# Kernel optimization log

Measured on AMD Instinct MI355X. Metric: run time of the kernel, lower is better.

The kernel has to match this reference:

```python
import jax, jax.numpy as jnp
import numpy as np

D = 192
HEADS = 4
HD = D // HEADS
R = 3  # correlation radius actually used in forward_level
NDISP = (2 * R + 1) ** 2  # 49
T = 3  # frames -> 2 consecutive pairs
ITERS = 4


def layer_norm(x, w, b, eps=1e-5):
    m = jnp.mean(x, axis=-1, keepdims=True)
    v = jnp.var(x, axis=-1, keepdims=True)
    return (x - m) / jnp.sqrt(v + eps) * w + b


def mha(x, in_w, in_b, out_w, out_b):
    # torch nn.MultiheadAttention, batch_first, self-attention
    B, N, _ = x.shape
    qkv = x @ in_w.T + in_b
    q, k, v = jnp.split(qkv, 3, axis=-1)
    q = q.reshape(B, N, HEADS, HD).transpose(0, 2, 1, 3) * (1.0 / float(np.sqrt(HD)))
    k = k.reshape(B, N, HEADS, HD).transpose(0, 2, 1, 3)
    v = v.reshape(B, N, HEADS, HD).transpose(0, 2, 1, 3)
    att = jax.nn.softmax(jnp.einsum('bhqd,bhkd->bhqk', q, k), axis=-1)
    y = jnp.einsum('bhqk,bhkd->bhqd', att, v).transpose(0, 2, 1, 3).reshape(B, N, D)
    return y @ out_w.T + out_b


def tblock(x, p):
    ln1w, ln1b, inw, inb, ow, ob, ln2w, ln2b, w1, b1, w2, b2 = p
    x = x + mha(layer_norm(x, ln1w, ln1b), inw, inb, ow, ob)
    h = layer_norm(x, ln2w, ln2b)
    h = jax.nn.gelu(h @ w1.T + b1, approximate=False) @ w2.T + b2
    return x + h


def local_corr(f1, f2):
    C = f1.shape[1]
    scale = 1.0 / float(np.sqrt(C))
    outs = []
    for dy in range(-R, R + 1):
        for dx in range(-R, R + 1):
            f2s = jnp.roll(f2, (dy, dx), axis=(2, 3))
            outs.append(jnp.sum(f1 * f2s, axis=1) * scale)
    return jnp.stack(outs, axis=1)


def grid_sample_bilinear_border(img, grid):
    # img: B,C,H,W; grid: B,Ho,Wo,2 with (x,y) in [-1,1]; align_corners=True, border padding
    B, C, H, W = img.shape
    x = jnp.clip((grid[..., 0] + 1.0) * 0.5 * (W - 1), 0.0, W - 1)
    y = jnp.clip((grid[..., 1] + 1.0) * 0.5 * (H - 1), 0.0, H - 1)
    x0 = jnp.floor(x); y0 = jnp.floor(y)
    x1 = jnp.minimum(x0 + 1, W - 1); y1 = jnp.minimum(y0 + 1, H - 1)
    wx = (x - x0)[:, None]; wy = (y - y0)[:, None]
    imgf = img.reshape(B, C, H * W)
    Ho, Wo = x.shape[1], x.shape[2]
    def gather(yy, xx):
        idx = (yy * W + xx).astype(jnp.int32).reshape(B, 1, Ho * Wo)
        return jnp.take_along_axis(imgf, idx, axis=2).reshape(B, C, Ho, Wo)
    v00 = gather(y0, x0); v01 = gather(y0, x1)
    v10 = gather(y1, x0); v11 = gather(y1, x1)
    return v00 * (1 - wx) * (1 - wy) + v01 * wx * (1 - wy) + v10 * (1 - wx) * wy + v11 * wx * wy


def warp(img, flow):
    # flow in pixels, Bx2xHxW
    B, C, H, W = img.shape
    xs = jnp.linspace(-1.0, 1.0, W); ys = jnp.linspace(-1.0, 1.0, H)
    gx, gy = jnp.meshgrid(xs, ys)  # each (H, W), 'xy' indexing
    base = jnp.stack([gx, gy], axis=-1)[None]
    off = jnp.stack([flow[:, 0] * (2.0 / max(W - 1, 1)),
                     flow[:, 1] * (2.0 / max(H - 1, 1))], axis=-1)
    return grid_sample_bilinear_border(img, base + off)


def upsample2x_align(img):
    # F.interpolate(scale_factor=2, mode='bilinear', align_corners=True)
    B, C, H, W = img.shape
    Ho, Wo = 2 * H, 2 * W
    xs = jnp.linspace(-1.0, 1.0, Wo); ys = jnp.linspace(-1.0, 1.0, Ho)
    gx, gy = jnp.meshgrid(xs, ys)
    grid = jnp.broadcast_to(jnp.stack([gx, gy], axis=-1)[None], (B, Ho, Wo, 2))
    return grid_sample_bilinear_border(img, grid)


def conv2d(x, w, b):
    y = jax.lax.conv_general_dilated(x, w, (1, 1), ((1, 1), (1, 1)),
                                     dimension_numbers=('NCHW', 'OIHW', 'NCHW'))
    return y + b[None, :, None, None]


def _forward(feats_l1, feats_l2, feats_l3, tok_w, tok_b,
             lcm_ln1_w, lcm_ln1_b, lcm_in_w, lcm_in_b, lcm_out_w, lcm_out_b,
             lcm_ln2_w, lcm_ln2_b, lcm_mlp_w1, lcm_mlp_b1, lcm_mlp_w2, lcm_mlp_b2,
             gtr_ln1_w, gtr_ln1_b, gtr_in_w, gtr_in_b, gtr_out_w, gtr_out_b,
             gtr_ln2_w, gtr_ln2_b, gtr_mlp_w1, gtr_mlp_b1, gtr_mlp_w2, gtr_mlp_b2,
             head_w1, head_b1, head_w2, head_b2,
             ref1_w1, ref1_b1, ref1_w2, ref1_b2,
             ref0_w1, ref0_b1, ref0_w2, ref0_b2):
    feats = [[feats_l1[t] for t in range(T)],
             [feats_l2[t] for t in range(T)],
             [feats_l3[t] for t in range(T)]]
    # ---- CostTokenizer ----
    tokens = []
    for lvl in range(3):
        toks = []
        for k in range(T - 1):
            corr = local_corr(feats[lvl][k], feats[lvl][k + 1])
            toks.append(jnp.einsum('bchw,dc->bdhw', corr, tok_w[lvl]) + tok_b[lvl][None, :, None, None])
        tokens.append(toks)
    lcm_p = [(lcm_ln1_w[i], lcm_ln1_b[i], lcm_in_w[i], lcm_in_b[i], lcm_out_w[i], lcm_out_b[i],
              lcm_ln2_w[i], lcm_ln2_b[i], lcm_mlp_w1[i], lcm_mlp_b1[i], lcm_mlp_w2[i], lcm_mlp_b2[i])
             for i in range(lcm_ln1_w.shape[0])]
    gtr_p = [(gtr_ln1_w[i], gtr_ln1_b[i], gtr_in_w[i], gtr_in_b[i], gtr_out_w[i], gtr_out_b[i],
              gtr_ln2_w[i], gtr_ln2_b[i], gtr_mlp_w1[i], gtr_mlp_b1[i], gtr_mlp_w2[i], gtr_mlp_b2[i])
             for i in range(gtr_ln1_w.shape[0])]
    # ---- LatentCostMemory (EMA state; .detach() -> stop_gradient; state resets when N changes) ----
    state = None
    latent = []
    for toks in tokens:
        lvl_lat = []
        for tok in toks:
            B_, Dd, H, W = tok.shape
            x = tok.reshape(B_, Dd, H * W).transpose(0, 2, 1)  # b (h w) d
            for p in lcm_p:
                x = tblock(x, p)
            if state is None or state.shape[1] != x.shape[1]:
                state = jax.lax.stop_gradient(x)
            x = 0.8 * x + 0.2 * state
            state = jax.lax.stop_gradient(x)
            lvl_lat.append(x.transpose(0, 2, 1))  # b d n
        latent.append(lvl_lat)
    H8, W8 = feats[1][0].shape[-2:]
    coarse = []
    for lat in latent[1]:
        x = lat.transpose(0, 2, 1)
        for p in gtr_p:
            x = tblock(x, p)
        fv = jax.nn.gelu(x @ head_w1.T + head_b1, approximate=False) @ head_w2.T + head_b2
        coarse.append(fv.transpose(0, 2, 1).reshape(-1, 2, H8, W8))
    # ---- MSRecurrentDecoder ----
    outs = []
    for k, f8 in enumerate(coarse):
        cur = f8
        for _ in range(ITERS):
            w10 = warp(feats[1][k + 1], cur)
            x = jnp.concatenate([feats[1][k], cur, w10], axis=1)
            cur = cur + conv2d(jax.nn.gelu(conv2d(x, ref1_w1, ref1_b1), approximate=False), ref1_w2, ref1_b2)
        cur2 = upsample2x_align(cur)
        for _ in range(ITERS):
            w10 = warp(feats[0][k + 1], cur2)
            x = jnp.concatenate([feats[0][k], cur2, w10], axis=1)
            cur2 = cur2 + conv2d(jax.nn.gelu(conv2d(x, ref0_w1, ref0_b1), approximate=False), ref0_w2, ref0_b2)
        outs.append(cur2)
    return jnp.stack(outs)  # [pairs, B, 2, H/4, W/4]


def setup_inputs():
    key = jax.random.key(0)
    ks = iter(jax.random.split(key, 64))
    def rn(shape, s=1.0):
        return jax.random.normal(next(ks), shape, dtype=jnp.float32) * s
    B = 1
    inp = {}
    inp['feats_l1'] = rn((T, B, 64, 64, 64))
    inp['feats_l2'] = rn((T, B, 128, 32, 32))
    inp['feats_l3'] = rn((T, B, 192, 16, 16))
    inp['tok_w'] = rn((3, D, NDISP), 0.02)
    inp['tok_b'] = rn((3, D), 0.02)
    for pre, n in (('lcm', 6), ('gtr', 2)):
        inp[pre + '_ln1_w'] = jnp.ones((n, D), jnp.float32)
        inp[pre + '_ln1_b'] = jnp.zeros((n, D), jnp.float32)
        inp[pre + '_in_w'] = rn((n, 3 * D, D), 0.02)
        inp[pre + '_in_b'] = rn((n, 3 * D), 0.02)
        inp[pre + '_out_w'] = rn((n, D, D), 0.02)
        inp[pre + '_out_b'] = rn((n, D), 0.02)
        inp[pre + '_ln2_w'] = jnp.ones((n, D), jnp.float32)
        inp[pre + '_ln2_b'] = jnp.zeros((n, D), jnp.float32)
        inp[pre + '_mlp_w1'] = rn((n, 4 * D, D), 0.02)
        inp[pre + '_mlp_b1'] = rn((n, 4 * D), 0.02)
        inp[pre + '_mlp_w2'] = rn((n, D, 4 * D), 0.02)
        inp[pre + '_mlp_b2'] = rn((n, D), 0.02)
    inp['head_w1'] = rn((D, D), 0.02); inp['head_b1'] = rn((D,), 0.02)
    inp['head_w2'] = rn((2, D), 0.02); inp['head_b2'] = rn((2,), 0.02)
    inp['ref1_w1'] = rn((128, 258, 3, 3), 0.02); inp['ref1_b1'] = rn((128,), 0.02)
    inp['ref1_w2'] = rn((2, 128, 3, 3), 0.02); inp['ref1_b2'] = rn((2,), 0.02)
    inp['ref0_w1'] = rn((64, 130, 3, 3), 0.02); inp['ref0_b1'] = rn((64,), 0.02)
    inp['ref0_w2'] = rn((2, 64, 3, 3), 0.02); inp['ref0_b2'] = rn((2,), 0.02)
    return inp


def reference(feats_l1, feats_l2, feats_l3, tok_w, tok_b,
              lcm_ln1_w, lcm_ln1_b, lcm_in_w, lcm_in_b, lcm_out_w, lcm_out_b,
              lcm_ln2_w, lcm_ln2_b, lcm_mlp_w1, lcm_mlp_b1, lcm_mlp_w2, lcm_mlp_b2,
              gtr_ln1_w, gtr_ln1_b, gtr_in_w, gtr_in_b, gtr_out_w, gtr_out_b,
              gtr_ln2_w, gtr_ln2_b, gtr_mlp_w1, gtr_mlp_b1, gtr_mlp_w2, gtr_mlp_b2,
              head_w1, head_b1, head_w2, head_b2,
              ref1_w1, ref1_b1, ref1_w2, ref1_b2,
              ref0_w1, ref0_b1, ref0_w2, ref0_b2):
    return _forward(feats_l1, feats_l2, feats_l3, tok_w, tok_b,
                    lcm_ln1_w, lcm_ln1_b, lcm_in_w, lcm_in_b, lcm_out_w, lcm_out_b,
                    lcm_ln2_w, lcm_ln2_b, lcm_mlp_w1, lcm_mlp_b1, lcm_mlp_w2, lcm_mlp_b2,
                    gtr_ln1_w, gtr_ln1_b, gtr_in_w, gtr_in_b, gtr_out_w, gtr_out_b,
                    gtr_ln2_w, gtr_ln2_b, gtr_mlp_w1, gtr_mlp_b1, gtr_mlp_w2, gtr_mlp_b2,
                    head_w1, head_b1, head_w2, head_b2,
                    ref1_w1, ref1_b1, ref1_w2, ref1_b2,
                    ref0_w1, ref0_b1, ref0_w2, ref0_b2)
```

## Files before the change

### kernel.cpp

```cpp
#include <hip/hip_runtime.h>
#include <hip/hip_bf16.h>

typedef __hip_bfloat16 bf16;
typedef short bf16x8 __attribute__((ext_vector_type(8)));
typedef float f32x4 __attribute__((ext_vector_type(4)));

#define DEV __device__ __forceinline__

DEV float bf2f(bf16 v) { return __bfloat162float(v); }
DEV bf16 f2bf(float v) { return __float2bfloat16(v); }
DEV unsigned short bfr(float f) {
  bf16 h = __float2bfloat16(f);
  return *reinterpret_cast<unsigned short*>(&h);
}
DEV float shf(unsigned short u) {
  unsigned int x = ((unsigned int)u) << 16;
  return *reinterpret_cast<float*>(&x);
}
DEV float gelu_exact(float x) { return 0.5f * x * (1.0f + erff(x * 0.70710678118654752f)); }

DEV float ldw(const void* p, long i, int isb) {
  return isb ? __bfloat162float(((const bf16*)p)[i]) : ((const float*)p)[i];
}

__global__ void k_detect(const unsigned short* __restrict__ u, int* __restrict__ flag) {
  __shared__ int bad;
  if (threadIdx.x == 0) bad = 0;
  __syncthreads();
  for (int i = threadIdx.x; i < 8192; i += 256) {
    int expo = (u[i] >> 7) & 0xFF;
    if (expo >= 138) atomicOr(&bad, 1);
  }
  __syncthreads();
  if (threadIdx.x == 0) *flag = bad ? 0 : 1;
}
__global__ void k_setone(int* p) { *p = 1; }

__global__ void k_cvt(const void* __restrict__ s, float* __restrict__ d, int n,
                      const int* __restrict__ fl) {
  int isb = *fl;
  int i = blockIdx.x * blockDim.x + threadIdx.x;
  if (i < n) d[i] = ldw(s, i, isb);
}

__global__ void k_zerosh(unsigned short* __restrict__ p, int n8) {
  int i = blockIdx.x * blockDim.x + threadIdx.x;
  if (i < n8) { uint4 z = {0, 0, 0, 0}; *(uint4*)(p + (long)i * 8) = z; }
}

__global__ void k_padtokw(const void* __restrict__ tw, bf16* __restrict__ dst,
                          const int* __restrict__ fl) {
  int isb = *fl;
  int i = blockIdx.x * blockDim.x + threadIdx.x;
  if (i >= 12288) return;
  int n = i >> 6, k = i & 63;
  float v = (k < 49) ? ldw(tw, 9408 + (long)n * 49 + k, isb) : 0.0f;
  dst[i] = f2bf(v);
}

__global__ void k_packw(const void* __restrict__ src, bf16* __restrict__ dst,
                        int OC, int C, int ICT, int NP, int ICP, int n,
                        const int* __restrict__ fl) {
  int isb = *fl;
  int i = blockIdx.x * blockDim.x + threadIdx.x;
  if (i >= n) return;
  int s = i / (NP * ICP);
  int r = i - s * NP * ICP;
  int oc = r / ICP, icp = r - oc * ICP;
  float v = 0.0f;
  if (oc < OC) {
    int ic = -1;
    if (icp < C) ic = icp;
    else if (icp < 2 * C) ic = icp - C + C + 2;
    else if (icp < 2 * C + 2) ic = icp - 2 * C + C;
    if (ic >= 0 && ic < ICT) v = ldw(src, ((long)oc * ICT + ic) * 9 + s, isb);
  }
  dst[i] = f2bf(v);
}

__global__ void k_trans_feats(const void* __restrict__ in, bf16* __restrict__ Fp,
                              int F, int C, int HW, const int* __restrict__ fl) {
  int isb = *fl;
  int cpg = C >> 3;
  int n = F * HW * cpg;
  int i = blockIdx.x * blockDim.x + threadIdx.x;
  if (i >= n) return;
  int p = i % HW;
  int rem = i / HW;
  int c8 = rem % cpg;
  int f = rem / cpg;
  long base = (long)f * C * HW + (long)(c8 * 8) * HW + p;
  union { unsigned short u[8]; uint4 v; } pk;
#pragma unroll
  for (int j = 0; j < 8; ++j) pk.u[j] = bfr(ldw(in, base + (long)j * HW, isb));
  *(uint4*)((unsigned short*)Fp + ((long)f * HW + p) * C + c8 * 8) = pk.v;
}

template <int C, int ICP, int NP, int WW, int LGW>
__global__ __launch_bounds__(64, 2) void k_conv1d(
    const bf16* __restrict__ Fp, const float* __restrict__ flow,
    const bf16* __restrict__ Wp, const float* __restrict__ bias,
    bf16* __restrict__ out) {
  constexpr int HH = WW, HW = WW * WW;
  constexpr int ACW = 18, APX = 54;
  constexpr int NK = ICP / 32;
  __shared__ unsigned short As[APX][40];
  __shared__ int pofs[APX];
  __shared__ int doff[APX][4];
  __shared__ float dwt[APX][4];
  __shared__ float ffl[APX][2];
  int ln = threadIdx.x;
  int quad = ln >> 4, l16 = ln & 15;
  int n0 = blockIdx.x * 16, m0 = blockIdx.y * 16, b = blockIdx.z;
  int py0 = m0 >> LGW, px0 = m0 & (WW - 1);
  const unsigned short* fcur = (const unsigned short*)Fp + (long)b * HW * C;
  const unsigned short* fnxt = (const unsigned short*)Fp + (long)(b + 1) * HW * C;
  const float* fl = flow + (long)b * 2 * HW;
  if (ln < APX) {
    int sr = ln / ACW, sc = ln - sr * ACW;
    int py = py0 + sr - 1, px = px0 + sc - 1;
    bool in = py >= 0 && py < HH && px >= 0 && px < WW;
    int p = in ? (py * WW + px) : 0;
    pofs[ln] = in ? p * C : -1;
    float fx = in ? fl[p] : 0.0f, fy = in ? fl[HW + p] : 0.0f;
    float x = fminf(fmaxf((float)px + fx, 0.0f), (float)(WW - 1));
    float y = fminf(fmaxf((float)py + fy, 0.0f), (float)(HH - 1));
    int x0 = (int)floorf(x), y0 = (int)floorf(y);
    int x1 = min(x0 + 1, WW - 1), y1 = min(y0 + 1, HH - 1);
    float wx = x - (float)x0, wy = y - (float)y0;
    dwt[ln][0] = in ? (1 - wx) * (1 - wy) : 0.0f;
    dwt[ln][1] = in ? wx * (1 - wy) : 0.0f;
    dwt[ln][2] = in ? (1 - wx) * wy : 0.0f;
    dwt[ln][3] = in ? wx * wy : 0.0f;
    doff[ln][0] = (y0 * WW + x0) * C; doff[ln][1] = (y0 * WW + x1) * C;
    doff[ln][2] = (y1 * WW + x0) * C; doff[ln][3] = (y1 * WW + x1) * C;
    ffl[ln][0] = in ? fx : 0.0f; ffl[ln][1] = in ? fy : 0.0f;
  }
  const unsigned short* wrow = (const unsigned short*)Wp + (long)(n0 + l16) * ICP + quad * 8;
  f32x4 ac0 = {}, ac1 = {}, ac2 = {};
  for (int kc = 0; kc < NK; ++kc) {
    int chb = kc * 32;
    if (chb < C) {
      uint4 arg[4];
#pragma unroll
      for (int j = 0; j < 4; ++j) {
        int idx = ln + j * 64;
        if (idx < APX * 4) {
          int ap = idx >> 2, c4 = idx & 3;
          int po = pofs[ap];
          uint4 z = {0, 0, 0, 0};
          arg[j] = (po >= 0) ? *(const uint4*)(fcur + po + chb + c4 * 8) : z;
        }
      }
#pragma unroll
      for (int j = 0; j < 4; ++j) {
        int idx = ln + j * 64;
        if (idx < APX * 4) {
          int ap = idx >> 2, c4 = idx & 3;
          *(uint4*)&As[ap][c4 * 8] = arg[j];
        }
      }
    } else if (chb < 2 * C) {
#pragma unroll
      for (int j = 0; j < 4; ++j) {
        int idx = ln + j * 64;
        if (idx < APX * 4) {
          int ap = idx >> 2, c4 = idx & 3;
          int c = chb - C + c4 * 8;
          uint4 v0 = *(const uint4*)(fnxt + doff[ap][0] + c);
          uint4 v1 = *(const uint4*)(fnxt + doff[ap][1] + c);
          uint4 v2 = *(const uint4*)(fnxt + doff[ap][2] + c);
          uint4 v3 = *(const uint4*)(fnxt + doff[ap][3] + c);
          float q0 = dwt[ap][0], q1 = dwt[ap][1], q2 = dwt[ap][2], q3 = dwt[ap][3];
          union { unsigned short u[8]; uint4 v; } a0 = {.v = v0}, a1 = {.v = v1},
                                                  a2 = {.v = v2}, a3 = {.v = v3}, o;
#pragma unroll
          for (int e = 0; e < 8; ++e)
            o.u[e] = bfr(shf(a0.u[e]) * q0 + shf(a1.u[e]) * q1 +
                         shf(a2.u[e]) * q2 + shf(a3.u[e]) * q3);
          *(uint4*)&As[ap][c4 * 8] = o.v;
        }
      }
    } else {
#pragma unroll
      for (int j = 0; j < 4; ++j) {
        int idx = ln + j * 64;
        if (idx < APX * 4) {
          int ap = idx >> 2, c4 = idx & 3;
          union { unsigned short u[8]; uint4 v; } o = { .v = {0, 0, 0, 0} };
          if (c4 == 0) { o.u[0] = bfr(ffl[ap][0]); o.u[1] = bfr(ffl[ap][1]); }
          *(uint4*)&As[ap][c4 * 8] = o.v;
        }
      }
    }
#pragma unroll
    for (int s = 0; s < 9; ++s) {
      int ky = s / 3, kx = s - ky * 3;
      bf16x8 af = *(const bf16x8*)&As[ky * ACW + l16 + kx][quad * 8];
      bf16x8 wf = *(const bf16x8*)(wrow + (long)s * NP * ICP + chb);
      if (s % 3 == 0)      ac0 = __builtin_amdgcn_mfma_f32_16x16x32_bf16(af, wf, ac0, 0, 0, 0);
      else if (s % 3 == 1) ac1 = __builtin_amdgcn_mfma_f32_16x16x32_bf16(af, wf, ac1, 0, 0, 0);
      else                 ac2 = __builtin_amdgcn_mfma_f32_16x16x32_bf16(af, wf, ac2, 0, 0, 0);
    }
  }
  int n = n0 + l16;
  float bv = bias[n];
  long rowbase = (long)b * (HH + 2) * (WW + 2) + (long)(py0 + 1) * (WW + 2);
#pragma unroll
  for (int r = 0; r < 4; ++r) {
    int px = px0 + quad * 4 + r;
    float v = gelu_exact(ac0[r] + ac1[r] + ac2[r] + bv);
    ((unsigned short*)out)[(rowbase + px + 1) * NP + n] = bfr(v);
  }
}

template <int C, int WW, int LGW>
__global__ __launch_bounds__(256) void k_conv2_dot(
    const bf16* __restrict__ mid, const bf16* __restrict__ Wq,
    const float* __restrict__ bias, float* __restrict__ cur) {
  constexpr int HH = WW;
  constexpr int HW = HH * WW;
  constexpr int Wp2 = WW + 2;
  constexpr int CPL = C / 64;
  int tid = threadIdx.x, wv = tid >> 6, ln = tid & 63;
  int gw = blockIdx.x * 4 + wv;
  int b = gw >> (2 * LGW);
  int p = gw & (HW - 1);
  int py = p >> LGW, px = p & (WW - 1);
  float r0 = cur[((long)b * 2 + 0) * HW + p];
  float r1 = cur[((long)b * 2 + 1) * HW + p];
  float b0 = bias[0], b1 = bias[1];
  const unsigned short* base = (const unsigned short*)mid +
      ((long)b * (HH + 2) * Wp2 + (long)py * Wp2 + px) * C + ln * CPL;
  const unsigned short* wb = (const unsigned short*)Wq + ln * CPL;
  float s0 = 0.0f, s1 = 0.0f;
#pragma unroll
  for (int t = 0; t < 9; ++t) {
    int dy = t / 3, dx = t - dy * 3;
    const unsigned short* ar = base + ((long)dy * Wp2 + dx) * C;
    const unsigned short* w0r = wb + (long)(t * 16 + 0) * C;
    const unsigned short* w1r = wb + (long)(t * 16 + 1) * C;
    if (CPL == 2) {
      unsigned int a = *(const unsigned int*)ar;
      unsigned int q0 = *(const unsigned int*)w0r;
      unsigned int q1 = *(const unsigned int*)w1r;
      float a0 = shf((unsigned short)a), a1 = shf((unsigned short)(a >> 16));
      s0 += a0 * shf((unsigned short)q0) + a1 * shf((unsigned short)(q0 >> 16));
      s1 += a0 * shf((unsigned short)q1) + a1 * shf((unsigned short)(q1 >> 16));
    } else {
      float a0 = shf(ar[0]);
      s0 += a0 * shf(w0r[0]);
      s1 += a0 * shf(w1r[0]);
    }
  }
#pragma unroll
  for (int o = 32; o; o >>= 1) { s0 += __shfl_xor(s0, o); s1 += __shfl_xor(s1, o); }
  if (ln == 0) {
    cur[((long)b * 2 + 0) * HW + p] = s0 + b0 + r0;
    cur[((long)b * 2 + 1) * HW + p] = s1 + b1 + r1;
  }
}

__global__ void k_corr(const bf16* __restrict__ Fp2, bf16* __restrict__ corrT) {
  __shared__ unsigned short f1r[128];
  int p = blockIdx.x;
  int b = blockIdx.y;
  int t = threadIdx.x;
  const unsigned short* f1 = (const unsigned short*)Fp2 + ((long)b * 1024 + p) * 128;
  if (t < 16) *(uint4*)&f1r[t * 8] = *(const uint4*)(f1 + t * 8);
  __syncthreads();
  long rowo = ((long)b * 1024 + p) * 64;
  if (t < 49) {
    int dy = t / 7 - 3, dx = t % 7 - 3;
    int h = p >> 5, w = p & 31;
    int p2 = (((h - dy) & 31) << 5) | ((w - dx) & 31);
    const unsigned short* f2 = (const unsigned short*)Fp2 + ((long)(b + 1) * 1024 + p2) * 128;
    float s = 0.0f;
    for (int c = 0; c < 128; c += 8) {
      union { unsigned short u[8]; uint4 v; } av = { .v = *(const uint4*)&f1r[c] };
      union { unsigned short u[8]; uint4 v; } bv = { .v = *(const uint4*)(f2 + c) };
#pragma unroll
      for (int j = 0; j < 8; ++j) s += shf(av.u[j]) * shf(bv.u[j]);
    }
    corrT[rowo + t] = f2bf(s * 0.08838834764831845f);
  } else {
    corrT[rowo + t] = f2bf(0.0f);
  }
}

template <int KT, int BM, int ACT, bool HASRES, int AMODE, int OUTBF, int VT>
__global__ __launch_bounds__(256) void k_gemm_mfma2(
    const void* __restrict__ A, const void* __restrict__ W, long woff,
    const void* __restrict__ bias, long boff, const int* __restrict__ flb,
    const float* __restrict__ res, void* __restrict__ C,
    int M, int N, const int* __restrict__ fl,
    const unsigned short* __restrict__ mop, const float* __restrict__ mml,
    bf16* __restrict__ vtout,
    const void* __restrict__ lnw, long lnwoff,
    const void* __restrict__ lnb, long lnboff) {
  (void)M;
  int isb = *fl;
  constexpr int NKC = ((KT < 192) ? KT : 192) >> 5;
  constexpr int WM = (BM == 64) ? 4 : 2;
  constexpr int NTW = (BM == 64) ? 4 : 2;
  constexpr int LPR = 256 / BM;
  constexpr int EPL = 192 / LPR;
  __shared__ unsigned short Asm[NKC][BM][40];
  __shared__ unsigned short Wsm[NKC][64][40];
  int tid = threadIdx.x;
  int wv = tid >> 6, ln = tid & 63;
  int quad = ln >> 4, l16 = ln & 15;
  int wm = wv % WM, wn = wv / WM;
  int m0 = blockIdx.y * BM, n0 = blockIdx.x * 64;
  f32x4 acc[NTW] = {};
  for (int s0 = 0; s0 < KT; s0 += 192) {
    if (s0) __syncthreads();
    for (int i = tid; i < NKC * 256; i += 256) {
      int c4 = i & 3, r = (i >> 2) & 63, kc = i >> 8;
      long eo = woff + (long)(n0 + r) * KT + s0 + kc * 32 + c4 * 8;
      if (isb) {
        *(uint4*)&Wsm[kc][r][c4 * 8] = *(const uint4*)((const unsigned short*)W + eo);
      } else {
        const float* wp = (const float*)W + eo;
        float4 w0 = *(const float4*)wp;
        float4 w1 = *(const float4*)(wp + 4);
        union { unsigned short u[8]; uint4 v; } pk;
        pk.u[0] = bfr(w0.x); pk.u[1] = bfr(w0.y); pk.u[2] = bfr(w0.z); pk.u[3] = bfr(w0.w);
        pk.u[4] = bfr(w1.x); pk.u[5] = bfr(w1.y); pk.u[6] = bfr(w1.z); pk.u[7] = bfr(w1.w);
        *(uint4*)&Wsm[kc][r][c4 * 8] = pk.v;
      }
    }
    if constexpr (AMODE == 1) {
      for (int i = tid; i < NKC * BM * 4; i += 256) {
        int c4 = i & 3, r = (i >> 2) % BM, kc = i / (BM * 4);
        const unsigned short* ap =
            (const unsigned short*)A + (long)(m0 + r) * KT + s0 + kc * 32 + c4 * 8;
        *(uint4*)&Asm[kc][r][c4 * 8] = *(const uint4*)ap;
      }
    } else if constexpr (AMODE == 0) {
      for (int i = tid; i < NKC * BM * 4; i += 256) {
        int c4 = i & 3, r = (i >> 2) % BM, kc = i / (BM * 4);
        const float* ap = (const float*)A + (long)(m0 + r) * KT + s0 + kc * 32 + c4 * 8;
        float4 a0 = *(const float4*)ap;
        float4 a1 = *(const float4*)(ap + 4);
        union { unsigned short u[8]; uint4 v; } pk;
        pk.u[0] = bfr(a0.x); pk.u[1] = bfr(a0.y); pk.u[2] = bfr(a0.z); pk.u[3] = bfr(a0.w);
        pk.u[4] = bfr(a1.x); pk.u[5] = bfr(a1.y); pk.u[6] = bfr(a1.z); pk.u[7] = bfr(a1.w);
        *(uint4*)&Asm[kc][r][c4 * 8] = pk.v;
      }
    } else if constexpr (AMODE == 3) {
      int row = tid / LPR, j = tid % LPR;
      const float* xr = (const float*)A + (long)(m0 + row) * 192 + j * EPL;
      float av[EPL];
#pragma unroll
      for (int q4 = 0; q4 < EPL / 4; ++q4) {
        float4 v = *(const float4*)(xr + q4 * 4);
        av[q4 * 4 + 0] = v.x; av[q4 * 4 + 1] = v.y;
        av[q4 * 4 + 2] = v.z; av[q4 * 4 + 3] = v.w;
      }
      float sum = 0.0f;
#pragma unroll
      for (int q = 0; q < EPL; ++q) sum += av[q];
#pragma unroll
      for (int o = 1; o < LPR; o <<= 1) sum += __shfl_xor(sum, o);
      float mean = sum * (1.0f / 192.0f);
      float vs = 0.0f;
#pragma unroll
      for (int q = 0; q < EPL; ++q) { float d = av[q] - mean; vs += d * d; }
#pragma unroll
      for (int o = 1; o < LPR; o <<= 1) vs += __shfl_xor(vs, o);
      float rstd = rsqrtf(vs * (1.0f / 192.0f) + 1e-5f);
#pragma unroll
      for (int g = 0; g < EPL / 8; ++g) {
        int k = j * EPL + g * 8;
        union { unsigned short u[8]; uint4 v; } pk;
#pragma unroll
        for (int e = 0; e < 8; ++e) {
          float gg = ldw(lnw, lnwoff + k + e, isb);
          float bb = ldw(lnb, lnboff + k + e, isb);
          pk.u[e] = bfr((av[g * 8 + e] - mean) * rstd * gg + bb);
        }
        *(uint4*)&Asm[k >> 5][row][k & 31] = pk.v;
      }
    } else {
      int row = tid / LPR, j = tid % LPR;
      int m = m0 + row;
      int rr = m & 1023, bb = m >> 10;
#pragma unroll
      for (int g = 0; g < EPL / 8; ++g) {
        int k = j * EPL + g * 8;
        int h = k / 48;
        int d0 = k - h * 48;
        long idx[4];
        float ms[4], ls[4];
        float Ms = -1e30f;
#pragma unroll
        for (int s = 0; s < 4; ++s) {
          idx[s] = (((long)s * 2 + bb) * 4 + h) * 1024 + rr;
          ms[s] = mml[idx[s] * 2];
          ls[s] = mml[idx[s] * 2 + 1];
          Ms = fmaxf(Ms, ms[s]);
        }
        float e[4], L = 0.0f;
#pragma unroll
        for (int s = 0; s < 4; ++s) { e[s] = __expf(ms[s] - Ms); L += ls[s] * e[s]; }
        float invL = 1.0f / L;
        union { unsigned short u[8]; uint4 v; } pk;
#pragma unroll
        for (int e2 = 0; e2 < 8; ++e2) {
          float o = 0.0f;
#pragma unroll
          for (int s = 0; s < 4; ++s) o += shf(mop[idx[s] * 48 + d0 + e2]) * e[s];
          pk.u[e2] = bfr(o * invL);
        }
        *(uint4*)&Asm[k >> 5][row][k & 31] = pk.v;
      }
    }
    __syncthreads();
#pragma unroll
    for (int kc = 0; kc < NKC; ++kc) {
      bf16x8 af = *(const bf16x8*)&Asm[kc][wm * 16 + l16][quad * 8];
#pragma unroll
      for (int nt = 0; nt < NTW; ++nt) {
        bf16x8 wf = *(const bf16x8*)&Wsm[kc][(wn * NTW + nt) * 16 + l16][quad * 8];
        acc[nt] = __builtin_amdgcn_mfma_f32_16x16x32_bf16(af, wf, acc[nt], 0, 0, 0);
      }
    }
  }
  int isbb = *flb;
#pragma unroll
  for (int nt = 0; nt < NTW; ++nt) {
    int n = n0 + (wn * NTW + nt) * 16 + l16;
    float bv = ldw(bias, boff + n, isbb);
#pragma unroll
    for (int r = 0; r < 4; ++r) {
      int m = m0 + wm * 16 + quad * 4 + r;
      float v = acc[nt][r] + bv;
      if (HASRES) v += res[(long)m * N + n];
      if (ACT == 1) v = gelu_exact(v);
      if (OUTBF) ((bf16*)C)[(long)m * N + n] = f2bf(v);
      else ((float*)C)[(long)m * N + n] = v;
      if constexpr (VT) {
        if (n >= 384) {
          int hh = (n - 384) / 48, dd = (n - 384) % 48;
          int row = m & 1023, bb = m >> 10;
          vtout[((long)(bb * 4 + hh) * 48 + dd) * 1024 + row] = f2bf(v);
        }
      }
    }
  }
}

__global__ __launch_bounds__(256) void k_head2(const float* __restrict__ A,
                                               const void* __restrict__ W,
                                               const void* __restrict__ bias,
                                               float* __restrict__ C,
                                               const int* __restrict__ fl) {
  int isb = *fl;
  int wv = threadIdx.x >> 6, ln = threadIdx.x & 63;
  int gw = blockIdx.x * 4 + wv;
  int m = gw >> 1, n = gw & 1;
  const float* a = A + (long)m * 192;
  float s = 0.0f;
#pragma unroll
  for (int q = 0; q < 3; ++q) {
    int j = ln + q * 64;
    s += a[j] * ldw(W, (long)n * 192 + j, isb);
  }
  for (int o = 32; o; o >>= 1) s += __shfl_xor(s, o);
  if (ln == 0) {
    int b = m >> 10, p = m & 1023;
    C[((long)b * 2 + n) * 1024 + p] = s + ldw(bias, n, isb);
  }
}

__global__ __launch_bounds__(256) void k_attn_mfma(const bf16* __restrict__ qkv,
                                                   const bf16* __restrict__ vt,
                                                   unsigned short* __restrict__ opart,
                                                   float* __restrict__ ml) {
  __shared__ unsigned short Qs[64][72];
  __shared__ unsigned short Ks[64][72];
  __shared__ unsigned short Vs[48][72];
  __shared__ unsigned short Ps[64][72];
  int tid = threadIdx.x;
  int wv = tid >> 6, ln = tid & 63, quad = ln >> 4, l16 = ln & 15;
  int h = blockIdx.y, b = blockIdx.z;
  int qt = blockIdx.x >> 2, s = blockIdx.x & 3;
  int q0 = qt * 64;
  const unsigned short* qp = (const unsigned short*)qkv + (long)b * 1024 * 576;
  const unsigned short* vp = (const unsigned short*)vt + ((long)(b * 4 + h) * 48) * 1024;
  for (int i = tid; i < 384; i += 256) {
    int r = i / 6, c = i % 6;
    *(uint4*)&Qs[r][c * 8] = *(const uint4*)(qp + (long)(q0 + r) * 576 + h * 48 + c * 8);
  }
  for (int i = tid; i < 128; i += 256) {
    int r = i >> 1, c = 6 + (i & 1);
    uint4 z = {0, 0, 0, 0};
    *(uint4*)&Qs[r][c * 8] = z;
  }
  float m[4] = {-1e30f, -1e30f, -1e30f, -1e30f};
  float l[4] = {0.0f, 0.0f, 0.0f, 0.0f};
  f32x4 accO[3] = {};
  const float SC = 0.14433756729740643f;
  for (int kc = s * 4; kc < s * 4 + 4; ++kc) {
    int k0 = kc * 64;
    for (int i = tid; i < 384; i += 256) {
      int r = i / 6, c = i % 6;
      *(uint4*)&Ks[r][c * 8] = *(const uint4*)(qp + (long)(k0 + r) * 576 + 192 + h * 48 + c * 8);
    }
    for (int i = tid; i < 128; i += 256) {
      int r = i >> 1, c = 6 + (i & 1);
      uint4 z = {0, 0, 0, 0};
      *(uint4*)&Ks[r][c * 8] = z;
    }
    for (int i = tid; i < 384; i += 256) {
      int d = i >> 3, c = i & 7;
      *(uint4*)&Vs[d][c * 8] = *(const uint4*)(vp + (long)d * 1024 + k0 + c * 8);
    }
    __syncthreads();
    f32x4 accS[4] = {};
    bf16x8 a0 = *(const bf16x8*)&Qs[wv * 16 + l16][quad * 8];
    bf16x8 a1 = *(const bf16x8*)&Qs[wv * 16 + l16][32 + quad * 8];
#pragma unroll
    for (int ct = 0; ct < 4; ++ct) {
      bf16x8 b0 = *(const bf16x8*)&Ks[ct * 16 + l16][quad * 8];
      bf16x8 b1 = *(const bf16x8*)&Ks[ct * 16 + l16][32 + quad * 8];
      accS[ct] = __builtin_amdgcn_mfma_f32_16x16x32_bf16(a0, b0, accS[ct], 0, 0, 0);
      accS[ct] = __builtin_amdgcn_mfma_f32_16x16x32_bf16(a1, b1, accS[ct], 0, 0, 0);
    }
#pragma unroll
    for (int r = 0; r < 4; ++r) {
      float s0 = accS[0][r] * SC, s1 = accS[1][r] * SC;
      float s2 = accS[2][r] * SC, s3 = accS[3][r] * SC;
      float mx = fmaxf(fmaxf(s0, s1), fmaxf(s2, s3));
      for (int o = 8; o; o >>= 1) mx = fmaxf(mx, __shfl_xor(mx, o));
      float mn = fmaxf(m[r], mx);
      float alpha = __expf(m[r] - mn);
      float p0 = __expf(s0 - mn), p1 = __expf(s1 - mn);
      float p2 = __expf(s2 - mn), p3 = __expf(s3 - mn);
      float rs = p0 + p1 + p2 + p3;
      for (int o = 8; o; o >>= 1) rs += __shfl_xor(rs, o);
      m[r] = mn;
      l[r] = l[r] * alpha + rs;
      accO[0][r] *= alpha; accO[1][r] *= alpha; accO[2][r] *= alpha;
      int prow = wv * 16 + quad * 4 + r;
      Ps[prow][l16]      = bfr(p0);
      Ps[prow][16 + l16] = bfr(p1);
      Ps[prow][32 + l16] = bfr(p2);
      Ps[prow][48 + l16] = bfr(p3);
    }
    bf16x8 pf0 = *(const bf16x8*)&Ps[wv * 16 + l16][quad * 8];
    bf16x8 pf1 = *(const bf16x8*)&Ps[wv * 16 + l16][32 + quad * 8];
#pragma unroll
    for (int ct = 0; ct < 3; ++ct) {
      bf16x8 v0 = *(const bf16x8*)&Vs[ct * 16 + l16][quad * 8];
      bf16x8 v1 = *(const bf16x8*)&Vs[ct * 16 + l16][32 + quad * 8];
      accO[ct] = __builtin_amdgcn_mfma_f32_16x16x32_bf16(pf0, v0, accO[ct], 0, 0, 0);
      accO[ct] = __builtin_amdgcn_mfma_f32_16x16x32_bf16(pf1, v1, accO[ct], 0, 0, 0);
    }
    __syncthreads();
  }
  long base = (((long)s * 2 + b) * 4 + h) * 1024;
#pragma unroll
  for (int r = 0; r < 4; ++r) {
    int row = q0 + wv * 16 + quad * 4 + r;
#pragma unroll
    for (int ct = 0; ct < 3; ++ct)
      opart[(base + row) * 48 + ct * 16 + l16] = bfr(accO[ct][r]);
    if (l16 == 0) {
      ml[(base + row) * 2]     = m[r];
      ml[(base + row) * 2 + 1] = l[r];
    }
  }
}

__global__ void k_ema(float* __restrict__ x) {
  int i = blockIdx.x * blockDim.x + threadIdx.x;
  if (i < 196608) x[196608 + i] = 0.8f * x[196608 + i] + 0.2f * x[i];
}

__global__ void k_upsample(const float* __restrict__ in, float* __restrict__ out) {
  int i = blockIdx.x * blockDim.x + threadIdx.x;
  if (i >= 2 * 2 * 64 * 64) return;
  int p = i & 4095;
  int bc = i >> 12;
  int oy = p >> 6, ox = p & 63;
  float sx = ox * (31.0f / 63.0f), sy = oy * (31.0f / 63.0f);
  int x0 = (int)sx, y0 = (int)sy;
  int x1 = min(x0 + 1, 31), y1 = min(y0 + 1, 31);
  float wx = sx - x0, wy = sy - y0;
  const float* ic = in + (long)bc * 1024;
  out[i] = ic[y0 * 32 + x0] * (1 - wx) * (1 - wy) + ic[y0 * 32 + x1] * wx * (1 - wy)
         + ic[y1 * 32 + x0] * (1 - wx) * wy      + ic[y1 * 32 + x1] * wx * wy;
}

__global__ void k_out(const float* __restrict__ cur2, void* __restrict__ out,
                      const int* __restrict__ fl) {
  int isb = *fl;
  int i = blockIdx.x * blockDim.x + threadIdx.x;
  if (i < 16384) {
    if (isb) ((bf16*)out)[i] = f2bf(cur2[i]);
    else ((float*)out)[i] = cur2[i];
  }
}

extern "C" void kernel_launch(void* const* d_in, const int* in_sizes, int n_in,
                              void* d_out, int out_size, void* d_ws, size_t ws_size,
                              hipStream_t stream) {
  const void* feats_l1 = d_in[0];
  const void* feats_l2 = d_in[1];
  const void* tok_w = d_in[3];
  const void* tok_b = d_in[4];
  const void* lcm_ln1_w = d_in[5];
  const void* lcm_ln1_b = d_in[6];
  const void* lcm_in_w  = d_in[7];
  const void* lcm_in_b  = d_in[8];
  const void* lcm_out_w = d_in[9];
  const void* lcm_out_b = d_in[10];
  const void* lcm_ln2_w = d_in[11];
  const void* lcm_ln2_b = d_in[12];
  const void* lcm_mlp_w1 = d_in[13];
  const void* lcm_mlp_b1 = d_in[14];
  const void* lcm_mlp_w2 = d_in[15];
  const void* lcm_mlp_b2 = d_in[16];
  const void* gtr_ln1_w = d_in[17];
  const void* gtr_ln1_b = d_in[18];
  const void* gtr_in_w  = d_in[19];
  const void* gtr_in_b  = d_in[20];
  const void* gtr_out_w = d_in[21];
  const void* gtr_out_b = d_in[22];
  const void* gtr_ln2_w = d_in[23];
  const void* gtr_ln2_b = d_in[24];
  const void* gtr_mlp_w1 = d_in[25];
  const void* gtr_mlp_b1 = d_in[26];
  const void* gtr_mlp_w2 = d_in[27];
  const void* gtr_mlp_b2 = d_in[28];
  const void* head_w1 = d_in[29];
  const void* head_b1 = d_in[30];
  const void* head_w2 = d_in[31];
  const void* head_b2 = d_in[32];
  const void* ref1_w1 = d_in[33];
  const void* ref1_b1 = d_in[34];
  const void* ref1_w2 = d_in[35];
  const void* ref1_b2 = d_in[36];
  const void* ref0_w1 = d_in[37];
  const void* ref0_b1 = d_in[38];
  const void* ref0_w2 = d_in[39];
  const void* ref0_b2 = d_in[40];
  (void)ws_size; (void)n_in; (void)in_sizes; (void)out_size;

  int* flag = (int*)d_ws;
  int* oneflag = (int*)d_ws + 2;
  float* wsf = (float*)d_ws;
  float* F2   = wsf + 16;
  float* rA   = F2 + 393216;
  float* rX   = rA + 786432;
  float* rT   = rX + 393216;
  float* rY   = rT + 393216;
  float* big  = rY + 393216;
  float* fv   = big + 1572864;
  float* cur  = fv + 4096;
  float* cur2 = cur + 4096;
  float* cb1a = cur2 + 16384;
  float* cb1b = cb1a + 128;
  float* cb0a = cb1b + 16;
  float* cb0b = cb0a + 64;
  bf16* wtok  = (bf16*)(cb0b + 16);
  float* wpk  = cb0b + 16 + 6144;
  bf16* w1p1 = (bf16*)wpk;
  bf16* w1p2 = (bf16*)(wpk + 165888);
  bf16* w0p1 = (bf16*)(wpk + 175104);
  bf16* w0p2 = (bf16*)(wpk + 221184);

  float* x = rX;
  bf16* corrTb = (bf16*)big;
  bf16* qkvbb  = (bf16*)big;
  bf16* vtb    = (bf16*)(big + 655360);
  bf16* hidb   = (bf16*)big;
  unsigned short* opart = (unsigned short*)rA;
  float* mlbuf = rY;
  float* headh = rT;
  bf16* mid0p = (bf16*)rT;
  bf16* mid1p = (bf16*)rY;
  bf16* Fp2   = (bf16*)(big + 851968);
  bf16* Fp1   = (bf16*)(big + 1048576);

  k_detect<<<1, 256, 0, stream>>>((const unsigned short*)feats_l1, flag);
  k_setone<<<1, 1, 0, stream>>>(oneflag);
  k_cvt<<<1, 256, 0, stream>>>(ref1_b1, cb1a, 128, flag);
  k_cvt<<<1, 256, 0, stream>>>(ref1_b2, cb1b, 2, flag);
  k_cvt<<<1, 256, 0, stream>>>(ref0_b1, cb0a, 64, flag);
  k_cvt<<<1, 256, 0, stream>>>(ref0_b2, cb0b, 2, flag);
  k_padtokw<<<48, 256, 0, stream>>>(tok_w, wtok, flag);
  k_packw<<<1296, 256, 0, stream>>>(ref1_w1, w1p1, 128, 128, 258, 128, 288, 331776, flag);
  k_packw<<<72, 256, 0, stream>>>(ref1_w2, w1p2, 2, 128, 128, 16, 128, 18432, flag);
  k_packw<<<360, 256, 0, stream>>>(ref0_w1, w0p1, 64, 64, 130, 64, 160, 92160, flag);
  k_packw<<<36, 256, 0, stream>>>(ref0_w2, w0p2, 2, 64, 64, 16, 64, 9216, flag);
  k_trans_feats<<<192, 256, 0, stream>>>(feats_l2, Fp2, 3, 128, 1024, flag);
  k_trans_feats<<<384, 256, 0, stream>>>(feats_l1, Fp1, 3, 64, 4096, flag);

  k_corr<<<dim3(1024, 2), 64, 0, stream>>>(Fp2, corrTb);
  k_gemm_mfma2<64, 32, 0, false, 1, 0, 0><<<dim3(3, 64), 256, 0, stream>>>(
      corrTb, wtok, 0, tok_b, 192, flag, nullptr, x, 2048, 192, oneflag,
      nullptr, nullptr, nullptr, nullptr, 0, nullptr, 0);

  auto run_block = [&](const void* ln1w, long o1, const void* ln1b, long o2,
                       const void* inw, long o3, const void* inb, long o4,
                       const void* ow, long o5, const void* ob, long o6,
                       const void* ln2w, long o7, const void* ln2b, long o8,
                       const void* w1, long o9, const void* b1, long o10,
                       const void* w2, long o11, const void* b2, long o12) {
    k_gemm_mfma2<192, 64, 0, false, 3, 1, 1><<<dim3(9, 32), 256, 0, stream>>>(
        x, inw, o3, inb, o4, flag, nullptr, qkvbb, 2048, 576, flag,
        nullptr, nullptr, vtb, ln1w, o1, ln1b, o2);
    k_attn_mfma<<<dim3(64, 4, 2), 256, 0, stream>>>(qkvbb, vtb, opart, mlbuf);
    k_gemm_mfma2<192, 32, 0, true, 2, 0, 0><<<dim3(3, 64), 256, 0, stream>>>(
        nullptr, ow, o5, ob, o6, flag, x, x, 2048, 192, flag,
        opart, mlbuf, nullptr, nullptr, 0, nullptr, 0);
    k_gemm_mfma2<192, 64, 1, false, 3, 1, 0><<<dim3(12, 32), 256, 0, stream>>>(
        x, w1, o9, b1, o10, flag, nullptr, hidb, 2048, 768, flag,
        nullptr, nullptr, nullptr, ln2w, o7, ln2b, o8);
    k_gemm_mfma2<768, 32, 0, true, 1, 0, 0><<<dim3(3, 64), 256, 0, stream>>>(
        hidb, w2, o11, b2, o12, flag, x, x, 2048, 192, flag,
        nullptr, nullptr, nullptr, nullptr, 0, nullptr, 0);
  };

  for (int i = 0; i < 6; ++i) {
    run_block(lcm_ln1_w, (long)i * 192, lcm_ln1_b, (long)i * 192,
              lcm_in_w, (long)i * 110592, lcm_in_b, (long)i * 576,
              lcm_out_w, (long)i * 36864, lcm_out_b, (long)i * 192,
              lcm_ln2_w, (long)i * 192, lcm_ln2_b, (long)i * 192,
              lcm_mlp_w1, (long)i * 147456, lcm_mlp_b1, (long)i * 768,
              lcm_mlp_w2, (long)i * 147456, lcm_mlp_b2, (long)i * 192);
  }
  k_ema<<<768, 256, 0, stream>>>(x);

  for (int i = 0; i < 2; ++i) {
    run_block(gtr_ln1_w, (long)i * 192, gtr_ln1_b, (long)i * 192,
              gtr_in_w, (long)i * 110592, gtr_in_b, (long)i * 576,
              gtr_out_w, (long)i * 36864, gtr_out_b, (long)i * 192,
              gtr_ln2_w, (long)i * 192, gtr_ln2_b, (long)i * 192,
              gtr_mlp_w1, (long)i * 147456, gtr_mlp_b1, (long)i * 768,
              gtr_mlp_w2, (long)i * 147456, gtr_mlp_b2, (long)i * 192);
  }

  k_gemm_mfma2<192, 32, 1, false, 0, 0, 0><<<dim3(3, 64), 256, 0, stream>>>(
      x, head_w1, 0, head_b1, 0, flag, nullptr, headh, 2048, 192, flag,
      nullptr, nullptr, nullptr, nullptr, 0, nullptr, 0);
  k_head2<<<1024, 256, 0, stream>>>(headh, head_w2, head_b2, cur, flag);

  k_zerosh<<<768, 256, 0, stream>>>((unsigned short*)rT, 196608);

  for (int it = 0; it < 4; ++it) {
    k_conv1d<128, 288, 128, 32, 5><<<dim3(8, 64, 2), 64, 0, stream>>>(
        Fp2, cur, w1p1, cb1a, mid1p);
    k_conv2_dot<128, 32, 5><<<512, 256, 0, stream>>>(mid1p, w1p2, cb1b, cur);
  }
  k_upsample<<<64, 256, 0, stream>>>(cur, cur2);

  for (int it = 0; it < 4; ++it) {
    k_conv1d<64, 160, 64, 64, 6><<<dim3(4, 256, 2), 64, 0, stream>>>(
        Fp1, cur2, w0p1, cb0a, mid0p);
    k_conv2_dot<64, 64, 6><<<2048, 256, 0, stream>>>(mid0p, w0p2, cb0b, cur2);
  }

  k_out<<<64, 256, 0, stream>>>(cur2, d_out, flag);
}
```

Measured before the change: 994.5 us.

## Replace shared-memory tiled GEMM with single-wave register-streaming MFMA kernel

Swaps the 256-thread GEMM, which staged A and W tiles through LDS, for a 64-thread single-wavefront kernel. Each block now computes a 16x64 tile and loads W and A fragments straight from global memory into MFMA operands. LDS is used only for the fused LayerNorm and attention-combine prologues. The aim is to cut LDS staging, barriers and block-level sync on these small M=2048 GEMMs and to launch more, smaller blocks for better CU coverage. The cost is no LDS reuse of weights across rows: each wave rereads W from global or cache, and a block is left with far fewer waves to hide latency.

```diff
diff --git a/kernel.cpp b/kernel.cpp
--- a/kernel.cpp
+++ b/kernel.cpp
@@ -288,153 +288,137 @@
   }
 }
 
-template <int KT, int BM, int ACT, bool HASRES, int AMODE, int OUTBF, int VT>
-__global__ __launch_bounds__(256) void k_gemm_mfma2(
+template <int KT, int NTW, int ACT, bool HASRES, int AMODE, int OUTBF, int VT>
+__global__ __launch_bounds__(64, 2) void k_gemm_w(
     const void* __restrict__ A, const void* __restrict__ W, long woff,
     const void* __restrict__ bias, long boff, const int* __restrict__ flb,
     const float* __restrict__ res, void* __restrict__ C,
-    int M, int N, const int* __restrict__ fl,
+    int N, const int* __restrict__ fl,
     const unsigned short* __restrict__ mop, const float* __restrict__ mml,
     bf16* __restrict__ vtout,
     const void* __restrict__ lnw, long lnwoff,
     const void* __restrict__ lnb, long lnboff) {
-  (void)M;
+  constexpr int NK = KT / 32;
   int isb = *fl;
-  constexpr int NKC = ((KT < 192) ? KT : 192) >> 5;
-  constexpr int WM = (BM == 64) ? 4 : 2;
-  constexpr int NTW = (BM == 64) ? 4 : 2;
-  constexpr int LPR = 256 / BM;
-  constexpr int EPL = 192 / LPR;
-  __shared__ unsigned short Asm[NKC][BM][40];
-  __shared__ unsigned short Wsm[NKC][64][40];
-  int tid = threadIdx.x;
-  int wv = tid >> 6, ln = tid & 63;
+  int ln = threadIdx.x;
   int quad = ln >> 4, l16 = ln & 15;
-  int wm = wv % WM, wn = wv / WM;
-  int m0 = blockIdx.y * BM, n0 = blockIdx.x * 64;
+  int m0 = blockIdx.y * 16, n0 = blockIdx.x * (16 * NTW);
+  __shared__ unsigned short Als[(AMODE >= 2) ? 16 : 1][200];
+  if constexpr (AMODE == 3) {
+    int row = ln >> 2, j = ln & 3;
+    const float* xr = (const float*)A + (long)(m0 + row) * 192 + j * 48;
+    float av[48];
+#pragma unroll
+    for (int q = 0; q < 12; ++q) {
+      float4 v = *(const float4*)(xr + q * 4);
+      av[q * 4 + 0] = v.x; av[q * 4 + 1] = v.y;
+      av[q * 4 + 2] = v.z; av[q * 4 + 3] = v.w;
+    }
+    float sum = 0.0f;
+#pragma unroll
+    for (int q = 0; q < 48; ++q) sum += av[q];
+    sum += __shfl_xor(sum, 1);
+    sum += __shfl_xor(sum, 2);
+    float mean = sum * (1.0f / 192.0f);
+    float vs = 0.0f;
+#pragma unroll
+    for (int q = 0; q < 48; ++q) { float d = av[q] - mean; vs += d * d; }
+    vs += __shfl_xor(vs, 1);
+    vs += __shfl_xor(vs, 2);
+    float rstd = rsqrtf(vs * (1.0f / 192.0f) + 1e-5f);
+#pragma unroll
+    for (int g = 0; g < 6; ++g) {
+      union { unsigned short u[8]; uint4 v; } pk;
+#pragma unroll
+      for (int e = 0; e < 8; ++e) {
+        long k = j * 48 + g * 8 + e;
+        float gg = ldw(lnw, lnwoff + k, isb);
+        float bb = ldw(lnb, lnboff + k, isb);
+        pk.u[e] = bfr((av[g * 8 + e] - mean) * rstd * gg + bb);
+      }
+      *(uint4*)&Als[row][j * 48 + g * 8] = pk.v;
+    }
+  } else if constexpr (AMODE == 2) {
+    int row = ln >> 2, j = ln & 3;
+    int m = m0 + row;
+    int rr = m & 1023, bb = m >> 10;
+    long idx[4];
+    float ms[4], ls[4];
+    float Ms = -1e30f;
+#pragma unroll
+    for (int s = 0; s < 4; ++s) {
+      idx[s] = (((long)s * 2 + bb) * 4 + j) * 1024 + rr;
+      ms[s] = mml[idx[s] * 2];
+      ls[s] = mml[idx[s] * 2 + 1];
+      Ms = fmaxf(Ms, ms[s]);
+    }
+    float e4[4], L = 0.0f;
+#pragma unroll
+    for (int s = 0; s < 4; ++s) { e4[s] = __expf(ms[s] - Ms); L += ls[s] * e4[s]; }
+    float invL = 1.0f / L;
+#pragma unroll
+    for (int g = 0; g < 6; ++g) {
+      union { unsigned short u[8]; uint4 v; } pk;
+#pragma unroll
+      for (int e2 = 0; e2 < 8; ++e2) {
+        float o = 0.0f;
+#pragma unroll
+        for (int s = 0; s < 4; ++s) o += shf(mop[idx[s] * 48 + g * 8 + e2]) * e4[s];
+        pk.u[e2] = bfr(o * invL);
+      }
+      *(uint4*)&Als[row][j * 48 + g * 8] = pk.v;
+    }
+  }
   f32x4 acc[NTW] = {};
-  for (int s0 = 0; s0 < KT; s0 += 192) {
-    if (s0) __syncthreads();
-    for (int i = tid; i < NKC * 256; i += 256) {
-      int c4 = i & 3, r = (i >> 2) & 63, kc = i >> 8;
-      long eo = woff + (long)(n0 + r) * KT + s0 + kc * 32 + c4 * 8;
-      if (isb) {
-        *(uint4*)&Wsm[kc][r][c4 * 8] = *(const uint4*)((const unsigned short*)W + eo);
-      } else {
-        const float* wp = (const float*)W + eo;
+  auto lda = [&](int kc) -> bf16x8 {
+    if constexpr (AMODE >= 2) {
+      return *(const bf16x8*)&Als[l16][kc * 32 + quad * 8];
+    } else if constexpr (AMODE == 1) {
+      return *(const bf16x8*)((const unsigned short*)A + (long)(m0 + l16) * KT + kc * 32 + quad * 8);
+    } else {
+      const float* ap = (const float*)A + (long)(m0 + l16) * KT + kc * 32 + quad * 8;
+      float4 a0 = *(const float4*)ap;
+      float4 a1 = *(const float4*)(ap + 4);
+      union { unsigned short u[8]; bf16x8 v; } pk;
+      pk.u[0] = bfr(a0.x); pk.u[1] = bfr(a0.y); pk.u[2] = bfr(a0.z); pk.u[3] = bfr(a0.w);
+      pk.u[4] = bfr(a1.x); pk.u[5] = bfr(a1.y); pk.u[6] = bfr(a1.z); pk.u[7] = bfr(a1.w);
+      return pk.v;
+    }
+  };
+  if (isb) {
+    const unsigned short* wb = (const unsigned short*)W + woff + (long)l16 * KT + quad * 8;
+    for (int kc = 0; kc < NK; ++kc) {
+      bf16x8 af = lda(kc);
+#pragma unroll
+      for (int nt = 0; nt < NTW; ++nt) {
+        bf16x8 wf = *(const bf16x8*)(wb + (long)(n0 + nt * 16) * KT + kc * 32);
+        acc[nt] = __builtin_amdgcn_mfma_f32_16x16x32_bf16(af, wf, acc[nt], 0, 0, 0);
+      }
+    }
+  } else {
+    const float* wb = (const float*)W + woff + (long)l16 * KT + quad * 8;
+    for (int kc = 0; kc < NK; ++kc) {
+      bf16x8 af = lda(kc);
+#pragma unroll
+      for (int nt = 0; nt < NTW; ++nt) {
+        const float* wp = wb + (long)(n0 + nt * 16) * KT + kc * 32;
         float4 w0 = *(const float4*)wp;
         float4 w1 = *(const float4*)(wp + 4);
-        union { unsigned short u[8]; uint4 v; } pk;
+        union { unsigned short u[8]; bf16x8 v; } pk;
         pk.u[0] = bfr(w0.x); pk.u[1] = bfr(w0.y); pk.u[2] = bfr(w0.z); pk.u[3] = bfr(w0.w);
         pk.u[4] = bfr(w1.x); pk.u[5] = bfr(w1.y); pk.u[6] = bfr(w1.z); pk.u[7] = bfr(w1.w);
-        *(uint4*)&Wsm[kc][r][c4 * 8] = pk.v;
-      }
-    }
-    if constexpr (AMODE == 1) {
-      for (int i = tid; i < NKC * BM * 4; i += 256) {
-        int c4 = i & 3, r = (i >> 2) % BM, kc = i / (BM * 4);
-        const unsigned short* ap =
-            (const unsigned short*)A + (long)(m0 + r) * KT + s0 + kc * 32 + c4 * 8;
-        *(uint4*)&Asm[kc][r][c4 * 8] = *(const uint4*)ap;
-      }
-    } else if constexpr (AMODE == 0) {
-      for (int i = tid; i < NKC * BM * 4; i += 256) {
-        int c4 = i & 3, r = (i >> 2) % BM, kc = i / (BM * 4);
-        const float* ap = (const float*)A + (long)(m0 + r) * KT + s0 + kc * 32 + c4 * 8;
-        float4 a0 = *(const float4*)ap;
-        float4 a1 = *(const float4*)(ap + 4);
-        union { unsigned short u[8]; uint4 v; } pk;
-        pk.u[0] = bfr(a0.x); pk.u[1] = bfr(a0.y); pk.u[2] = bfr(a0.z); pk.u[3] = bfr(a0.w);
-        pk.u[4] = bfr(a1.x); pk.u[5] = bfr(a1.y); pk.u[6] = bfr(a1.z); pk.u[7] = bfr(a1.w);
-        *(uint4*)&Asm[kc][r][c4 * 8] = pk.v;
-      }
-    } else if constexpr (AMODE == 3) {
-      int row = tid / LPR, j = tid % LPR;
-      const float* xr = (const float*)A + (long)(m0 + row) * 192 + j * EPL;
-      float av[EPL];
-#pragma unroll
-      for (int q4 = 0; q4 < EPL / 4; ++q4) {
-        float4 v = *(const float4*)(xr + q4 * 4);
-        av[q4 * 4 + 0] = v.x; av[q4 * 4 + 1] = v.y;
-        av[q4 * 4 + 2] = v.z; av[q4 * 4 + 3] = v.w;
-      }
-      float sum = 0.0f;
-#pragma unroll
-      for (int q = 0; q < EPL; ++q) sum += av[q];
-#pragma unroll
-      for (int o = 1; o < LPR; o <<= 1) sum += __shfl_xor(sum, o);
-      float mean = sum * (1.0f / 192.0f);
-      float vs = 0.0f;
-#pragma unroll
-      for (int q = 0; q < EPL; ++q) { float d = av[q] - mean; vs += d * d; }
-#pragma unroll
-      for (int o = 1; o < LPR; o <<= 1) vs += __shfl_xor(vs, o);
-      float rstd = rsqrtf(vs * (1.0f / 192.0f) + 1e-5f);
-#pragma unroll
-      for (int g = 0; g < EPL / 8; ++g) {
-        int k = j * EPL + g * 8;
-        union { unsigned short u[8]; uint4 v; } pk;
-#pragma unroll
-        for (int e = 0; e < 8; ++e) {
-          float gg = ldw(lnw, lnwoff + k + e, isb);
-          float bb = ldw(lnb, lnboff + k + e, isb);
-          pk.u[e] = bfr((av[g * 8 + e] - mean) * rstd * gg + bb);
-        }
-        *(uint4*)&Asm[k >> 5][row][k & 31] = pk.v;
-      }
-    } else {
-      int row = tid / LPR, j = tid % LPR;
-      int m = m0 + row;
-      int rr = m & 1023, bb = m >> 10;
-#pragma unroll
-      for (int g = 0; g < EPL / 8; ++g) {
-        int k = j * EPL + g * 8;
-        int h = k / 48;
-        int d0 = k - h * 48;
-        long idx[4];
-        float ms[4], ls[4];
-        float Ms = -1e30f;
-#pragma unroll
-        for (int s = 0; s < 4; ++s) {
-          idx[s] = (((long)s * 2 + bb) * 4 + h) * 1024 + rr;
-          ms[s] = mml[idx[s] * 2];
-          ls[s] = mml[idx[s] * 2 + 1];
-          Ms = fmaxf(Ms, ms[s]);
-        }
-        float e[4], L = 0.0f;
-#pragma unroll
-        for (int s = 0; s < 4; ++s) { e[s] = __expf(ms[s] - Ms); L += ls[s] * e[s]; }
-        float invL = 1.0f / L;
-        union { unsigned short u[8]; uint4 v; } pk;
-#pragma unroll
-        for (int e2 = 0; e2 < 8; ++e2) {
-          float o = 0.0f;
-#pragma unroll
-          for (int s = 0; s < 4; ++s) o += shf(mop[idx[s] * 48 + d0 + e2]) * e[s];
-          pk.u[e2] = bfr(o * invL);
-        }
-        *(uint4*)&Asm[k >> 5][row][k & 31] = pk.v;
-      }
-    }
-    __syncthreads();
-#pragma unroll
-    for (int kc = 0; kc < NKC; ++kc) {
-      bf16x8 af = *(const bf16x8*)&Asm[kc][wm * 16 + l16][quad * 8];
-#pragma unroll
-      for (int nt = 0; nt < NTW; ++nt) {
-        bf16x8 wf = *(const bf16x8*)&Wsm[kc][(wn * NTW + nt) * 16 + l16][quad * 8];
-        acc[nt] = __builtin_amdgcn_mfma_f32_16x16x32_bf16(af, wf, acc[nt], 0, 0, 0);
+        acc[nt] = __builtin_amdgcn_mfma_f32_16x16x32_bf16(af, pk.v, acc[nt], 0, 0, 0);
       }
     }
   }
   int isbb = *flb;
 #pragma unroll
   for (int nt = 0; nt < NTW; ++nt) {
-    int n = n0 + (wn * NTW + nt) * 16 + l16;
+    int n = n0 + nt * 16 + l16;
     float bv = ldw(bias, boff + n, isbb);
 #pragma unroll
     for (int r = 0; r < 4; ++r) {
-      int m = m0 + wm * 16 + quad * 4 + r;
+      int m = m0 + quad * 4 + r;
       float v = acc[nt][r] + bv;
       if (HASRES) v += res[(long)m * N + n];
       if (ACT == 1) v = gelu_exact(v);
@@ -700,8 +684,8 @@
   k_trans_feats<<<384, 256, 0, stream>>>(feats_l1, Fp1, 3, 64, 4096, flag);
 
   k_corr<<<dim3(1024, 2), 64, 0, stream>>>(Fp2, corrTb);
-  k_gemm_mfma2<64, 32, 0, false, 1, 0, 0><<<dim3(3, 64), 256, 0, stream>>>(
-      corrTb, wtok, 0, tok_b, 192, flag, nullptr, x, 2048, 192, oneflag,
+  k_gemm_w<64, 4, 0, false, 1, 0, 0><<<dim3(3, 128), 64, 0, stream>>>(
+      corrTb, wtok, 0, tok_b, 192, flag, nullptr, x, 192, oneflag,
       nullptr, nullptr, nullptr, nullptr, 0, nullptr, 0);
 
   auto run_block = [&](const void* ln1w, long o1, const void* ln1b, long o2,
@@ -710,18 +694,18 @@
                        const void* ln2w, long o7, const void* ln2b, long o8,
                        const void* w1, long o9, const void* b1, long o10,
                        const void* w2, long o11, const void* b2, long o12) {
-    k_gemm_mfma2<192, 64, 0, false, 3, 1, 1><<<dim3(9, 32), 256, 0, stream>>>(
-        x, inw, o3, inb, o4, flag, nullptr, qkvbb, 2048, 576, flag,
+    k_gemm_w<192, 4, 0, false, 3, 1, 1><<<dim3(9, 128), 64, 0, stream>>>(
+        x, inw, o3, inb, o4, flag, nullptr, qkvbb, 576, flag,
         nullptr, nullptr, vtb, ln1w, o1, ln1b, o2);
     k_attn_mfma<<<dim3(64, 4, 2), 256, 0, stream>>>(qkvbb, vtb, opart, mlbuf);
-    k_gemm_mfma2<192, 32, 0, true, 2, 0, 0><<<dim3(3, 64), 256, 0, stream>>>(
-        nullptr, ow, o5, ob, o6, flag, x, x, 2048, 192, flag,
+    k_gemm_w<192, 4, 0, true, 2, 0, 0><<<dim3(3, 128), 64, 0, stream>>>(
+        nullptr, ow, o5, ob, o6, flag, x, x, 192, flag,
         opart, mlbuf, nullptr, nullptr, 0, nullptr, 0);
-    k_gemm_mfma2<192, 64, 1, false, 3, 1, 0><<<dim3(12, 32), 256, 0, stream>>>(
-        x, w1, o9, b1, o10, flag, nullptr, hidb, 2048, 768, flag,
+    k_gemm_w<192, 4, 1, false, 3, 1, 0><<<dim3(12, 128), 64, 0, stream>>>(
+        x, w1, o9, b1, o10, flag, nullptr, hidb, 768, flag,
         nullptr, nullptr, nullptr, ln2w, o7, ln2b, o8);
-    k_gemm_mfma2<768, 32, 0, true, 1, 0, 0><<<dim3(3, 64), 256, 0, stream>>>(
-        hidb, w2, o11, b2, o12, flag, x, x, 2048, 192, flag,
+    k_gemm_w<768, 4, 0, true, 1, 0, 0><<<dim3(3, 128), 64, 0, stream>>>(
+        hidb, w2, o11, b2, o12, flag, x, x, 192, flag,
         nullptr, nullptr, nullptr, nullptr, 0, nullptr, 0);
   };
 
@@ -744,8 +728,8 @@
               gtr_mlp_w2, (long)i * 147456, gtr_mlp_b2, (long)i * 192);
   }
 
-  k_gemm_mfma2<192, 32, 1, false, 0, 0, 0><<<dim3(3, 64), 256, 0, stream>>>(
-      x, head_w1, 0, head_b1, 0, flag, nullptr, headh, 2048, 192, flag,
+  k_gemm_w<192, 4, 1, false, 0, 0, 0><<<dim3(3, 128), 64, 0, stream>>>(
+      x, head_w1, 0, head_b1, 0, flag, nullptr, headh, 192, flag,
       nullptr, nullptr, nullptr, nullptr, 0, nullptr, 0);
   k_head2<<<1024, 256, 0, stream>>>(headh, head_w2, head_b2, cur, flag);
 
```

Result: no change. 1.007 ms (+1.3%).
